# Optimization experiments

Measured on AMD Instinct MI355X. Metric: run time of the kernel, lower is better.

The kernel has to match this reference:

```python
import jax, jax.numpy as jnp
import numpy as np

INPUT_SIZE = 512
OUTPUT_SIZE = 512
BATCH = 65536
HIDDEN = [256, 128, 64, 32]


def _linear_params(key, fan_in, fan_out):
    # torch nn.Linear default init: U(-1/sqrt(fan_in), 1/sqrt(fan_in))
    kw, kb = jax.random.split(key)
    bound = 1.0 / np.sqrt(fan_in)
    w = jax.random.uniform(kw, (fan_out, fan_in), jnp.float32, -bound, bound)
    b = jax.random.uniform(kb, (fan_out,), jnp.float32, -bound, bound)
    return w, b


def setup_inputs() -> dict:
    key = jax.random.key(0)
    ks = jax.random.split(key, 6)
    x = jax.random.normal(ks[0], (BATCH, INPUT_SIZE), jnp.float32)
    dims = [INPUT_SIZE] + HIDDEN + [OUTPUT_SIZE]
    inp = {"x": x}
    for i in range(5):
        w, b = _linear_params(ks[i + 1], dims[i], dims[i + 1])
        inp[f"w{i+1}"] = w
        inp[f"b{i+1}"] = b
    return inp


def reference(x, w1, b1, w2, b2, w3, b3, w4, b4, w5, b5):
    sig = jax.nn.sigmoid
    # in_size = number of nonzero entries in row 0 (replaces per-element python loop)
    in_size = jnp.count_nonzero(x[0])  # traced int scalar
    h = sig(x @ w1.T + b1)
    h = sig(h @ w2.T + b2)
    h = sig(h @ w3.T + b3)
    h = sig(h @ w4.T + b4)
    y = h @ w5.T + b5  # [B, OUTPUT_SIZE]
    # out has shape [B, INPUT_SIZE]; out[:, :in_size] = y[:, :in_size]
    # (INPUT_SIZE == OUTPUT_SIZE here, so a prefix mask suffices)
    mask = jnp.arange(INPUT_SIZE) < in_size  # [INPUT_SIZE]
    out = jnp.where(mask[None, :], y, jnp.zeros((), y.dtype))
    return out
```

## Files before the change

kernel.cpp:

```cpp
#include <hip/hip_runtime.h>
#include <hip/hip_bf16.h>
#include <stdint.h>

typedef __attribute__((ext_vector_type(4))) float f32x4;
typedef __attribute__((ext_vector_type(4))) unsigned int u32x4;
typedef __attribute__((ext_vector_type(8))) short short8;

#define MFMA16(a, b, c) __builtin_amdgcn_mfma_f32_16x16x32_bf16((a), (b), (c), 0, 0, 0)

__device__ __forceinline__ uint16_t f2bf(float f) {
  __hip_bfloat16 h = __float2bfloat16(f);
  return __builtin_bit_cast(uint16_t, h);
}

__device__ __forceinline__ short8 cvt8(f32x4 a, f32x4 b) {
  short8 r;
  r[0] = (short)f2bf(a[0]); r[1] = (short)f2bf(a[1]);
  r[2] = (short)f2bf(a[2]); r[3] = (short)f2bf(a[3]);
  r[4] = (short)f2bf(b[0]); r[5] = (short)f2bf(b[1]);
  r[6] = (short)f2bf(b[2]); r[7] = (short)f2bf(b[3]);
  return r;
}

template <int RB>
__device__ __forceinline__ int swzoff(int row, int bcol) {
  constexpr int SLM = (((RB / 16) < 8 ? (RB / 16) : 8)) - 1;
  return row * RB + (bcol ^ ((row & SLM) << 4));
}

template <int RB>
__device__ __forceinline__ short8 lds_a(const uint16_t* buf, int row0, int k0, int lane) {
  int r = row0 + (lane & 15);
  int bcol = (k0 + ((lane >> 4) << 3)) * 2;
  u32x4 raw = *(const u32x4*)((const char*)buf + swzoff<RB>(r, bcol));
  return __builtin_bit_cast(short8, raw);
}

__device__ __forceinline__ short8 load_frag_f32(const float* M, int ld, int r0, int k0, int lane) {
  const float* p = M + (size_t)(r0 + (lane & 15)) * ld + (k0 + ((lane >> 4) << 3));
  f32x4 a = *(const f32x4*)p;
  f32x4 b = *(const f32x4*)(p + 4);
  return cvt8(a, b);
}

__device__ __forceinline__ short8 load_b_pk(const char* base, int f, int lane) {
  u32x4 raw = *(const u32x4*)(base + (((size_t)f * 64 + lane) << 4));
  return __builtin_bit_cast(short8, raw);
}

template <bool P>
__device__ __forceinline__ short8 bfrag(const char* wp, const float* W, int K,
                                        int f0, int ntg, int KT, int kt, int lane) {
  if constexpr (P) {
    return load_b_pk(wp, f0 + ntg * KT + kt, lane);
  } else {
    return load_frag_f32(W, K, ntg * 16, kt * 32, lane);
  }
}

__global__ void pack_kernel(const float* __restrict__ w1, const float* __restrict__ w2,
                            const float* __restrict__ w3, const float* __restrict__ w4,
                            const float* __restrict__ w5, char* __restrict__ ws) {
  int b = blockIdx.x, lane = threadIdx.x;
  const float* W;
  int K, f0;
  if (b < 256)      { W = w1; K = 512; f0 = 0; }
  else if (b < 320) { W = w2; K = 256; f0 = 256; }
  else if (b < 336) { W = w3; K = 128; f0 = 320; }
  else if (b < 340) { W = w4; K = 64;  f0 = 336; }
  else              { W = w5; K = 32;  f0 = 340; }
  int f = b - f0;
  int KT = K / 32;
  int nt = f / KT, kt = f % KT;
  short8 r = load_frag_f32(W, K, nt * 16, kt * 32, lane);
  *(u32x4*)(ws + (((size_t)b * 64 + lane) << 4)) = __builtin_bit_cast(u32x4, r);
}

__device__ __forceinline__ void glds_chunk(const float* xbase, char* sring, int c,
                                           int wid, int lane) {
  char* sb = sring + (size_t)(c & 3) * 8192;
#pragma unroll
  for (int i = 0; i < 2; ++i) {
    int p = wid * 128 + i * 64 + lane;
    int r = p >> 3;
    int q = (p & 7) ^ (r & 7);
    const float* src = xbase + (size_t)r * 512 + c * 32 + q * 4;
    __builtin_amdgcn_global_load_lds(
        (const __attribute__((address_space(1))) unsigned int*)src,
        (__attribute__((address_space(3))) unsigned int*)(sb + ((size_t)(wid * 128 + i * 64) << 4)),
        16, 0, 0);
  }
}

__device__ __forceinline__ short8 lds_a_f32(const char* sb, int row0, int lane) {
  int r = row0 + (lane & 15);
  int g = (lane >> 4) << 1;
  int sw = r & 7;
  const char* rowp = sb + (size_t)r * 128;
  f32x4 a = *(const f32x4*)(rowp + ((g ^ sw) << 4));
  f32x4 b = *(const f32x4*)(rowp + (((g + 1) ^ sw) << 4));
  return cvt8(a, b);
}

#define WAITBAR(VN)                                          \
  asm volatile("s_waitcnt vmcnt(" #VN ")" ::: "memory");     \
  __builtin_amdgcn_s_barrier();

#define KSTEP(C, VN)                                                          \
  {                                                                           \
    WAITBAR(VN);                                                              \
    if ((C) < 13) glds_chunk(xbase, smem, (C) + 3, wid, lane);                \
    short8 bfr[4];                                                            \
    _Pragma("unroll") for (int nt = 0; nt < 4; ++nt)                          \
        bfr[nt] = bfrag<P>(wp, w1, 512, 0, wid * 4 + nt, 16, (C), lane);      \
    char* sc = smem + (size_t)((C) & 3) * 8192;                               \
    _Pragma("unroll") for (int m = 0; m < 4; ++m) {                           \
      short8 a = lds_a_f32(sc, m * 16, lane);                                 \
      _Pragma("unroll") for (int nt = 0; nt < 4; ++nt)                        \
          acc[m][nt] = MFMA16(a, bfr[nt], acc[m][nt]);                        \
    }                                                                         \
  }

template <bool P>
__global__ __launch_bounds__(256, 3) void mlp5_kernel(
    const float* __restrict__ x,
    const float* __restrict__ w1, const float* __restrict__ b1,
    const float* __restrict__ w2, const float* __restrict__ b2,
    const float* __restrict__ w3, const float* __restrict__ b3,
    const float* __restrict__ w4, const float* __restrict__ b4,
    const float* __restrict__ w5, const float* __restrict__ b5,
    const char* __restrict__ wp, float* __restrict__ out) {
  __shared__ __align__(16) char smem[48 * 1024];
  uint16_t* H1 = (uint16_t*)smem;
  uint16_t* H2 = (uint16_t*)(smem + 32 * 1024);
  uint16_t* H3 = (uint16_t*)smem;
  uint16_t* H4 = (uint16_t*)(smem + 8 * 1024);

  const int tid = threadIdx.x;
  const int lane = tid & 63;
  const int wid = tid >> 6;
  const int row0 = blockIdx.x * 64;
  const int lr = (lane >> 4) << 2;
  const int lc = lane & 15;

  int in_size = 0;
#pragma unroll
  for (int j = 0; j < 8; ++j) {
    float v = x[j * 64 + lane];
    in_size += (int)__popcll(__ballot(v != 0.f));
  }

  const float* xbase = x + (size_t)row0 * 512;

  f32x4 acc[4][4];
#pragma unroll
  for (int m = 0; m < 4; ++m)
#pragma unroll
    for (int n = 0; n < 4; ++n) acc[m][n] = (f32x4){0.f, 0.f, 0.f, 0.f};

  glds_chunk(xbase, smem, 0, wid, lane);
  glds_chunk(xbase, smem, 1, wid, lane);
  glds_chunk(xbase, smem, 2, wid, lane);

  KSTEP(0, 4)  KSTEP(1, 4)  KSTEP(2, 4)  KSTEP(3, 4)
  KSTEP(4, 4)  KSTEP(5, 4)  KSTEP(6, 4)  KSTEP(7, 4)
  KSTEP(8, 4)  KSTEP(9, 4)  KSTEP(10, 4) KSTEP(11, 4)
  KSTEP(12, 4) KSTEP(13, 4) KSTEP(14, 2) KSTEP(15, 0)

  short8 bfr2[2][8];
#pragma unroll
  for (int n = 0; n < 2; ++n)
#pragma unroll
    for (int kt = 0; kt < 8; ++kt)
      bfr2[n][kt] = bfrag<P>(wp, w2, 256, 256, wid * 2 + n, 8, kt, lane);

  __syncthreads();

#pragma unroll
  for (int n = 0; n < 4; ++n) {
    const int ncol = wid * 64 + n * 16;
    const float bv = b1[ncol + lc];
#pragma unroll
    for (int m = 0; m < 4; ++m)
#pragma unroll
      for (int i = 0; i < 4; ++i) {
        float v = acc[m][n][i] + bv;
        v = 1.f / (1.f + __expf(-v));
        *(uint16_t*)((char*)H1 + swzoff<512>(m * 16 + lr + i, (ncol + lc) * 2)) = f2bf(v);
      }
  }
  __syncthreads();

  {
    f32x4 acc2[4][2];
#pragma unroll
    for (int m = 0; m < 4; ++m)
#pragma unroll
      for (int n = 0; n < 2; ++n) acc2[m][n] = (f32x4){0.f, 0.f, 0.f, 0.f};
#pragma unroll
    for (int m = 0; m < 4; ++m) {
#pragma unroll
      for (int kt = 0; kt < 8; ++kt) {
        short8 afr = lds_a<512>(H1, m * 16, kt * 32, lane);
        acc2[m][0] = MFMA16(afr, bfr2[0][kt], acc2[m][0]);
        acc2[m][1] = MFMA16(afr, bfr2[1][kt], acc2[m][1]);
      }
    }
    short8 bfr3[4];
#pragma unroll
    for (int kt = 0; kt < 4; ++kt)
      bfr3[kt] = bfrag<P>(wp, w3, 128, 320, wid, 4, kt, lane);
    __syncthreads();
#pragma unroll
    for (int n = 0; n < 2; ++n) {
      const int ncol = wid * 32 + n * 16;
      const float bv = b2[ncol + lc];
#pragma unroll
      for (int m = 0; m < 4; ++m)
#pragma unroll
        for (int i = 0; i < 4; ++i) {
          float v = acc2[m][n][i] + bv;
          v = 1.f / (1.f + __expf(-v));
          *(uint16_t*)((char*)H2 + swzoff<256>(m * 16 + lr + i, (ncol + lc) * 2)) = f2bf(v);
        }
    }
    __syncthreads();

    f32x4 acc3[4];
#pragma unroll
    for (int m = 0; m < 4; ++m) acc3[m] = (f32x4){0.f, 0.f, 0.f, 0.f};
#pragma unroll
    for (int m = 0; m < 4; ++m)
#pragma unroll
      for (int kt = 0; kt < 4; ++kt) {
        short8 afr = lds_a<256>(H2, m * 16, kt * 32, lane);
        acc3[m] = MFMA16(afr, bfr3[kt], acc3[m]);
      }
    short8 bfr4[2];
#pragma unroll
    for (int kt = 0; kt < 2; ++kt)
      bfr4[kt] = bfrag<P>(wp, w4, 64, 336, wid & 1, 2, kt, lane);
    {
      const int ncol = wid * 16;
      const float bv = b3[ncol + lc];
#pragma unroll
      for (int m = 0; m < 4; ++m)
#pragma unroll
        for (int i = 0; i < 4; ++i) {
          float v = acc3[m][i] + bv;
          v = 1.f / (1.f + __expf(-v));
          *(uint16_t*)((char*)H3 + swzoff<128>(m * 16 + lr + i, (ncol + lc) * 2)) = f2bf(v);
        }
    }
    __syncthreads();

    const int wm = wid >> 1, wn = wid & 1;
    f32x4 acc4[2];
#pragma unroll
    for (int mt = 0; mt < 2; ++mt) acc4[mt] = (f32x4){0.f, 0.f, 0.f, 0.f};
#pragma unroll
    for (int mt = 0; mt < 2; ++mt)
#pragma unroll
      for (int kt = 0; kt < 2; ++kt) {
        short8 afr = lds_a<128>(H3, wm * 32 + mt * 16, kt * 32, lane);
        acc4[mt] = MFMA16(afr, bfr4[kt], acc4[mt]);
      }
    short8 bfr5[8];
#pragma unroll
    for (int nt = 0; nt < 8; ++nt)
      bfr5[nt] = bfrag<P>(wp, w5, 32, 340, wid * 8 + nt, 1, 0, lane);
    {
      const int ncol = wn * 16;
      const float bv = b4[ncol + lc];
#pragma unroll
      for (int mt = 0; mt < 2; ++mt)
#pragma unroll
        for (int i = 0; i < 4; ++i) {
          float v = acc4[mt][i] + bv;
          v = 1.f / (1.f + __expf(-v));
          *(uint16_t*)((char*)H4 + swzoff<64>(wm * 32 + mt * 16 + lr + i, (ncol + lc) * 2)) = f2bf(v);
        }
    }
    __syncthreads();

#pragma unroll
    for (int m = 0; m < 4; ++m) {
      short8 afr = lds_a<64>(H4, m * 16, 0, lane);
#pragma unroll
      for (int nt = 0; nt < 8; ++nt) {
        f32x4 av = MFMA16(afr, bfr5[nt], ((f32x4){0.f, 0.f, 0.f, 0.f}));
        const int col = wid * 128 + nt * 16 + lc;
        const float bv = b5[col];
        const bool keep = col < in_size;
#pragma unroll
        for (int i = 0; i < 4; ++i) {
          float v = keep ? (av[i] + bv) : 0.f;
          out[(size_t)(row0 + m * 16 + lr + i) * 512 + col] = v;
        }
      }
    }
  }
}

extern "C" void kernel_launch(void* const* d_in, const int* in_sizes, int n_in,
                              void* d_out, int out_size, void* d_ws, size_t ws_size,
                              hipStream_t stream) {
  const float* x  = (const float*)d_in[0];
  const float* w1 = (const float*)d_in[1];
  const float* b1 = (const float*)d_in[2];
  const float* w2 = (const float*)d_in[3];
  const float* b2 = (const float*)d_in[4];
  const float* w3 = (const float*)d_in[5];
  const float* b3 = (const float*)d_in[6];
  const float* w4 = (const float*)d_in[7];
  const float* b4 = (const float*)d_in[8];
  const float* w5 = (const float*)d_in[9];
  const float* b5 = (const float*)d_in[10];
  float* out = (float*)d_out;

  dim3 grid(65536 / 64);
  dim3 block(256);
  const bool packed = ws_size >= (size_t)(372 * 1024);
  if (packed) {
    pack_kernel<<<372, 64, 0, stream>>>(w1, w2, w3, w4, w5, (char*)d_ws);
    mlp5_kernel<true><<<grid, block, 0, stream>>>(x, w1, b1, w2, b2, w3, b3, w4, b4,
                                                  w5, b5, (const char*)d_ws, out);
  } else {
    mlp5_kernel<false><<<grid, block, 0, stream>>>(x, w1, b1, w2, b2, w3, b3, w4, b4,
                                                   w5, b5, nullptr, out);
  }
}
```

Measured before the change: 77.51 us.

## Prefetch W1 fragments one step ahead, shrink LDS for 4 blocks/CU, fast sigmoid

The layer-1 B fragments are now double-buffered in registers and loaded one K-step ahead, which hides global weight latency behind the MFMAs; the vmcnt waits are adjusted to match. The shared memory buffer shrinks from 48KB to 32KB by re-aliasing H2, H3 and H4, and launch bounds go from 3 to 4 blocks per CU to raise occupancy. The sigmoid division becomes a hardware reciprocal. In exchange, register pressure rises under the tighter launch bound, which risks spills, and the reciprocal gives slightly less accurate sigmoid values.

```diff
diff --git a/kernel.cpp b/kernel.cpp
--- a/kernel.cpp
+++ b/kernel.cpp
@@ -11,6 +11,10 @@
 __device__ __forceinline__ uint16_t f2bf(float f) {
   __hip_bfloat16 h = __float2bfloat16(f);
   return __builtin_bit_cast(uint16_t, h);
+}
+
+__device__ __forceinline__ float fast_sigmoid(float v) {
+  return __builtin_amdgcn_rcpf(1.f + __expf(-v));
 }
 
 __device__ __forceinline__ short8 cvt8(f32x4 a, f32x4 b) {
@@ -109,20 +113,23 @@
 #define KSTEP(C, VN)                                                          \
   {                                                                           \
     WAITBAR(VN);                                                              \
+    if ((C) < 15) {                                                           \
+      _Pragma("unroll") for (int nt = 0; nt < 4; ++nt)                        \
+          bfr[((C) + 1) & 1][nt] =                                            \
+              bfrag<P>(wp, w1, 512, 0, wid * 4 + nt, 16, (C) + 1, lane);      \
+    }                                                                         \
+    __builtin_amdgcn_sched_barrier(0);                                        \
     if ((C) < 13) glds_chunk(xbase, smem, (C) + 3, wid, lane);                \
-    short8 bfr[4];                                                            \
-    _Pragma("unroll") for (int nt = 0; nt < 4; ++nt)                          \
-        bfr[nt] = bfrag<P>(wp, w1, 512, 0, wid * 4 + nt, 16, (C), lane);      \
     char* sc = smem + (size_t)((C) & 3) * 8192;                               \
     _Pragma("unroll") for (int m = 0; m < 4; ++m) {                           \
       short8 a = lds_a_f32(sc, m * 16, lane);                                 \
       _Pragma("unroll") for (int nt = 0; nt < 4; ++nt)                        \
-          acc[m][nt] = MFMA16(a, bfr[nt], acc[m][nt]);                        \
+          acc[m][nt] = MFMA16(a, bfr[(C) & 1][nt], acc[m][nt]);               \
     }                                                                         \
   }
 
 template <bool P>
-__global__ __launch_bounds__(256, 3) void mlp5_kernel(
+__global__ __launch_bounds__(256, 4) void mlp5_kernel(
     const float* __restrict__ x,
     const float* __restrict__ w1, const float* __restrict__ b1,
     const float* __restrict__ w2, const float* __restrict__ b2,
@@ -130,11 +137,11 @@
     const float* __restrict__ w4, const float* __restrict__ b4,
     const float* __restrict__ w5, const float* __restrict__ b5,
     const char* __restrict__ wp, float* __restrict__ out) {
-  __shared__ __align__(16) char smem[48 * 1024];
+  __shared__ __align__(16) char smem[32 * 1024];
   uint16_t* H1 = (uint16_t*)smem;
-  uint16_t* H2 = (uint16_t*)(smem + 32 * 1024);
-  uint16_t* H3 = (uint16_t*)smem;
-  uint16_t* H4 = (uint16_t*)(smem + 8 * 1024);
+  uint16_t* H2 = (uint16_t*)smem;
+  uint16_t* H3 = (uint16_t*)(smem + 16 * 1024);
+  uint16_t* H4 = (uint16_t*)(smem + 24 * 1024);
 
   const int tid = threadIdx.x;
   const int lane = tid & 63;
@@ -158,14 +165,18 @@
 #pragma unroll
     for (int n = 0; n < 4; ++n) acc[m][n] = (f32x4){0.f, 0.f, 0.f, 0.f};
 
+  short8 bfr[2][4];
   glds_chunk(xbase, smem, 0, wid, lane);
+#pragma unroll
+  for (int nt = 0; nt < 4; ++nt)
+    bfr[0][nt] = bfrag<P>(wp, w1, 512, 0, wid * 4 + nt, 16, 0, lane);
   glds_chunk(xbase, smem, 1, wid, lane);
   glds_chunk(xbase, smem, 2, wid, lane);
 
-  KSTEP(0, 4)  KSTEP(1, 4)  KSTEP(2, 4)  KSTEP(3, 4)
-  KSTEP(4, 4)  KSTEP(5, 4)  KSTEP(6, 4)  KSTEP(7, 4)
-  KSTEP(8, 4)  KSTEP(9, 4)  KSTEP(10, 4) KSTEP(11, 4)
-  KSTEP(12, 4) KSTEP(13, 4) KSTEP(14, 2) KSTEP(15, 0)
+  KSTEP(0, 4)  KSTEP(1, 2)  KSTEP(2, 2)  KSTEP(3, 2)
+  KSTEP(4, 2)  KSTEP(5, 2)  KSTEP(6, 2)  KSTEP(7, 2)
+  KSTEP(8, 2)  KSTEP(9, 2)  KSTEP(10, 2) KSTEP(11, 2)
+  KSTEP(12, 2) KSTEP(13, 2) KSTEP(14, 0) KSTEP(15, 0)
 
   short8 bfr2[2][8];
 #pragma unroll
@@ -184,8 +195,7 @@
     for (int m = 0; m < 4; ++m)
 #pragma unroll
       for (int i = 0; i < 4; ++i) {
-        float v = acc[m][n][i] + bv;
-        v = 1.f / (1.f + __expf(-v));
+        float v = fast_sigmoid(acc[m][n][i] + bv);
         *(uint16_t*)((char*)H1 + swzoff<512>(m * 16 + lr + i, (ncol + lc) * 2)) = f2bf(v);
       }
   }
@@ -219,8 +229,7 @@
       for (int m = 0; m < 4; ++m)
 #pragma unroll
         for (int i = 0; i < 4; ++i) {
-          float v = acc2[m][n][i] + bv;
-          v = 1.f / (1.f + __expf(-v));
+          float v = fast_sigmoid(acc2[m][n][i] + bv);
           *(uint16_t*)((char*)H2 + swzoff<256>(m * 16 + lr + i, (ncol + lc) * 2)) = f2bf(v);
         }
     }
@@ -247,8 +256,7 @@
       for (int m = 0; m < 4; ++m)
 #pragma unroll
         for (int i = 0; i < 4; ++i) {
-          float v = acc3[m][i] + bv;
-          v = 1.f / (1.f + __expf(-v));
+          float v = fast_sigmoid(acc3[m][i] + bv);
           *(uint16_t*)((char*)H3 + swzoff<128>(m * 16 + lr + i, (ncol + lc) * 2)) = f2bf(v);
         }
     }
@@ -276,8 +284,7 @@
       for (int mt = 0; mt < 2; ++mt)
 #pragma unroll
         for (int i = 0; i < 4; ++i) {
-          float v = acc4[mt][i] + bv;
-          v = 1.f / (1.f + __expf(-v));
+          float v = fast_sigmoid(acc4[mt][i] + bv);
           *(uint16_t*)((char*)H4 + swzoff<64>(wm * 32 + mt * 16 + lr + i, (ncol + lc) * 2)) = f2bf(v);
         }
     }
```

Result: slower. 94.16 us (+21.5%).
